# Optimization experiments

Hardware: AMD Instinct MI355X
Metric: run time of the kernel (lower is better)

## Reference

```python
import jax, jax.numpy as jnp
import numpy as np

KEY_CH = 256

def _conv1x1(w, b, t):
    # 1x1 conv with BN folded: t [B,Cin,N] -> [B,Cout,N]
    return jnp.einsum('oc,bcn->bon', w, t) + b[None, :, None]

def _conv1x1_relu(w, b, t):
    return jax.nn.relu(_conv1x1(w, b, t))

def setup_inputs() -> dict:
    key = jax.random.key(0)
    ks = jax.random.split(key, 12)
    B, C, H, W = 4, 512, 128, 128
    d = {}
    d['feat'] = jax.random.normal(ks[0], (B, C, H, W), jnp.float32)
    d['prob'] = jax.random.normal(ks[1], (B, 20, H, W), jnp.float32)  # unused by forward (overwritten)
    s = 0.02
    d['wp1'] = jax.random.normal(ks[2], (KEY_CH, C), jnp.float32) * s
    d['bp1'] = jnp.zeros((KEY_CH,), jnp.float32)
    d['wp2'] = jax.random.normal(ks[3], (KEY_CH, KEY_CH), jnp.float32) * s
    d['bp2'] = jnp.zeros((KEY_CH,), jnp.float32)
    d['wo1'] = jax.random.normal(ks[4], (KEY_CH, C), jnp.float32) * s
    d['bo1'] = jnp.zeros((KEY_CH,), jnp.float32)
    d['wo2'] = jax.random.normal(ks[5], (KEY_CH, KEY_CH), jnp.float32) * s
    d['bo2'] = jnp.zeros((KEY_CH,), jnp.float32)
    d['wd'] = jax.random.normal(ks[6], (KEY_CH, C), jnp.float32) * s
    d['bd'] = jnp.zeros((KEY_CH,), jnp.float32)
    d['wu'] = jax.random.normal(ks[7], (C, KEY_CH), jnp.float32) * s
    d['bu'] = jnp.zeros((C,), jnp.float32)
    d['wout'] = jax.random.normal(ks[8], (512, 2 * C), jnp.float32) * s
    d['bout'] = jnp.zeros((512,), jnp.float32)
    return d


def reference(feat, prob, wp1, bp1, wp2, bp2, wo1, bo1, wo2, bo2, wd, bd, wu, bu, wout, bout):
    B, C, H, W = feat.shape
    x = feat.reshape(B, C, H * W)  # [B,C,N]
    # prob = upsample_bilinear(feat, (H,W)) == feat (identity resize); prob arg is dead.
    # SpatialGather (scale=1): softmax over spatial, weighted pool of features.
    pw = jax.nn.softmax(x, axis=-1)                     # [B,K,N], K == C here
    context = jnp.einsum('bkn,bcn->bck', pw, x)         # [B,C,K] proxy features
    # ObjectAttentionBlock2D
    q = _conv1x1_relu(wp2, bp2, _conv1x1_relu(wp1, bp1, x))        # [B,key,N]
    k = _conv1x1_relu(wo2, bo2, _conv1x1_relu(wo1, bo1, context))  # [B,key,K]
    v = _conv1x1_relu(wd, bd, context)                             # [B,key,K]
    sim = jnp.einsum('bdn,bdk->bnk', q, k) * (KEY_CH ** -0.5)      # [B,N,K]
    sim = jax.nn.softmax(sim, axis=-1)
    ctx = jnp.einsum('bnk,bdk->bdn', sim, v)                       # [B,key,N]
    ctx = _conv1x1_relu(wu, bu, ctx)                               # [B,C,N]
    # SpatialOCR: concat + 1x1 conv + BN + ReLU (dropout identity at eval)
    out = _conv1x1_relu(wout, bout, jnp.concatenate([ctx, x], axis=1))  # [B,out,N]
    return out.reshape(B, -1, H, W)
```

## Files before the change

### kernel.cpp

```cpp
#include <hip/hip_runtime.h>

typedef unsigned int u32;
typedef unsigned short u16;
typedef short s16x8 __attribute__((ext_vector_type(8)));
typedef float f32x4 __attribute__((ext_vector_type(4)));

__device__ __forceinline__ u16 f2bf(float f) {
  u32 u = __float_as_uint(f);
  u32 r = (u + 0x7fffu + ((u >> 16) & 1u)) >> 16;
  return (u16)r;
}

template <int MODE>
__device__ __forceinline__ uint4 pack8(const float* p, float2 st) {
  float4 f0 = *(const float4*)p;
  float4 f1 = *(const float4*)(p + 4);
  float v[8] = {f0.x, f0.y, f0.z, f0.w, f1.x, f1.y, f1.z, f1.w};
  if (MODE == 2) {
#pragma unroll
    for (int j = 0; j < 8; ++j) v[j] = __expf(v[j] - st.x) * st.y;
  }
  uint4 o;
  o.x = (u32)f2bf(v[0]) | ((u32)f2bf(v[1]) << 16);
  o.y = (u32)f2bf(v[2]) | ((u32)f2bf(v[3]) << 16);
  o.z = (u32)f2bf(v[4]) | ((u32)f2bf(v[5]) << 16);
  o.w = (u32)f2bf(v[6]) | ((u32)f2bf(v[7]) << 16);
  return o;
}

__device__ __forceinline__ void g2l16(u16* lds, const u16* g) {
  __builtin_amdgcn_global_load_lds(
      (const __attribute__((address_space(1))) void*)g,
      (__attribute__((address_space(3))) void*)lds, 16, 0, 0);
}

__global__ __launch_bounds__(256) void row_softmax_bf16(
    const float* __restrict__ feat, u16* __restrict__ expx,
    u16* __restrict__ xbf) {
  const long long row = blockIdx.x;
  const float* xp = feat + row * 16384;
  const int tid = threadIdx.x, wv = tid >> 6, ln = tid & 63;
  __shared__ float red[4];
  float4 v[16];
  float mx = -1e30f;
#pragma unroll
  for (int p = 0; p < 16; ++p) {
    v[p] = *(const float4*)(xp + tid * 4 + p * 1024);
    mx = fmaxf(mx, fmaxf(fmaxf(v[p].x, v[p].y), fmaxf(v[p].z, v[p].w)));
  }
  u16* bp = xbf + row * 16384;
#pragma unroll
  for (int p = 0; p < 16; ++p) {
    uint2 ow;
    ow.x = (u32)f2bf(v[p].x) | ((u32)f2bf(v[p].y) << 16);
    ow.y = (u32)f2bf(v[p].z) | ((u32)f2bf(v[p].w) << 16);
    *(uint2*)(bp + tid * 4 + p * 1024) = ow;
  }
  for (int o = 32; o; o >>= 1) mx = fmaxf(mx, __shfl_xor(mx, o, 64));
  if (!ln) red[wv] = mx;
  __syncthreads();
  mx = fmaxf(fmaxf(red[0], red[1]), fmaxf(red[2], red[3]));
  __syncthreads();
  float s = 0.f;
#pragma unroll
  for (int p = 0; p < 16; ++p) {
    v[p].x = __expf(v[p].x - mx);
    v[p].y = __expf(v[p].y - mx);
    v[p].z = __expf(v[p].z - mx);
    v[p].w = __expf(v[p].w - mx);
    s += v[p].x + v[p].y + v[p].z + v[p].w;
  }
  for (int o = 32; o; o >>= 1) s += __shfl_xor(s, o, 64);
  if (!ln) red[wv] = s;
  __syncthreads();
  const float inv = 1.f / (red[0] + red[1] + red[2] + red[3]);
  u16* op = expx + row * 16384;
#pragma unroll
  for (int p = 0; p < 16; ++p) {
    uint2 ow;
    ow.x = (u32)f2bf(v[p].x * inv) | ((u32)f2bf(v[p].y * inv) << 16);
    ow.y = (u32)f2bf(v[p].z * inv) | ((u32)f2bf(v[p].w * inv) << 16);
    *(uint2*)(op + tid * 4 + p * 1024) = ow;
  }
}

__global__ __launch_bounds__(256) void transpose_x(const u16* __restrict__ xbf,
                                                   u16* __restrict__ catT) {
  __shared__ u16 t[32][33];
  const int b = blockIdx.z;
  const int c0 = blockIdx.y << 5, n0 = blockIdx.x << 5;
  const int tx = threadIdx.x & 31, ty = threadIdx.x >> 5;
  const u16* fb = xbf + (long long)b * 512 * 16384;
#pragma unroll
  for (int i = 0; i < 32; i += 8)
    t[ty + i][tx] = fb[(long long)(c0 + ty + i) * 16384 + n0 + tx];
  __syncthreads();
  u16* ob = catT + (long long)b * 16384 * 1024 + 512;
#pragma unroll
  for (int i = 0; i < 32; i += 8)
    ob[(long long)(n0 + ty + i) * 1024 + c0 + tx] = t[tx][ty + i];
}

__global__ __launch_bounds__(256) void cvt_weights(
    const float* __restrict__ w0, const float* __restrict__ w1,
    const float* __restrict__ w2, const float* __restrict__ w3,
    const float* __restrict__ w4, const float* __restrict__ w5,
    const float* __restrict__ w6, u16* __restrict__ dst) {
  const long long i = (long long)blockIdx.x * 256 + threadIdx.x;
  const float* s;
  long long off;
  if (i < 131072) { s = w0; off = 0; }
  else if (i < 196608) { s = w1; off = 131072; }
  else if (i < 327680) { s = w2; off = 196608; }
  else if (i < 393216) { s = w3; off = 327680; }
  else if (i < 524288) { s = w4; off = 393216; }
  else if (i < 655360) { s = w5; off = 524288; }
  else { s = w6; off = 655360; }
  dst[i] = f2bf(s[i - off]);
}

template <int ACT, int BIAS, int SPLITK, int F32OUT>
__global__ __launch_bounds__(512, 1) void gemm256_nt(
    const u16* __restrict__ A, long long sA, int lda,
    const u16* __restrict__ B, long long sB, int ldb,
    void* __restrict__ C, long long sC, int ldc,
    const float* __restrict__ bias, int K, int kchunk) {
  __shared__ __align__(16) u16 As[2][256 * 64];
  __shared__ __align__(16) u16 Bs[2][256 * 64];
  const int tid = threadIdx.x;
  const int wid = tid >> 6, ln = tid & 63;
  const int bz = blockIdx.z;
  const int batch = SPLITK ? (bz >> SPLITK) : bz;
  const int chunk = SPLITK ? (bz & ((1 << SPLITK) - 1)) : 0;
  const long long tm = (long long)blockIdx.y << 8;
  const long long tn = (long long)blockIdx.x << 8;
  const int srow = wid * 8 + (ln >> 3);
  const int scl = ((ln & 7) ^ (ln >> 3)) << 3;
  const long long koff = SPLITK ? (long long)chunk * kchunk : 0;
  const u16* Ab = A + (long long)batch * sA + koff + scl;
  const u16* Bb = B + (long long)batch * sB + koff + scl;
  const u16* rA[4];
  const u16* rB[4];
#pragma unroll
  for (int s = 0; s < 4; ++s) {
    rA[s] = Ab + (tm + s * 64 + srow) * (long long)lda;
    rB[s] = Bb + (tn + s * 64 + srow) * (long long)ldb;
  }
  auto stage = [&](int buf, int kk) {
#pragma unroll
    for (int s = 0; s < 4; ++s) {
      g2l16(&As[buf][s * 4096 + wid * 512], rA[s] + kk);
      g2l16(&Bs[buf][s * 4096 + wid * 512], rB[s] + kk);
    }
  };
  const int fr = ln & 15, fq = ln >> 4;
  const int wm8 = wid >> 2;
  const int wn8 = wid & 3;
  const int arow = (wm8 * 128 + fr) * 64;
  const int brow = (wn8 * 64 + fr) * 64;
  const int ax = fr & 7;
  const int c0 = ((fq ^ ax) << 3);
  const int c1 = c0 ^ 32;
  f32x4 acc[8][4] = {};
  const int nt = (SPLITK ? kchunk : K) >> 6;
  stage(0, 0);
  asm volatile("s_waitcnt vmcnt(0)" ::: "memory");
  asm volatile("s_barrier" ::: "memory");
  for (int t = 0; t < nt; ++t) {
    const int cur = t & 1;
    if (t + 1 < nt) stage(cur ^ 1, (t + 1) << 6);
    s16x8 bfr[4][2];
#pragma unroll
    for (int nf = 0; nf < 4; ++nf) {
      bfr[nf][0] = *(const s16x8*)&Bs[cur][brow + nf * 1024 + c0];
      bfr[nf][1] = *(const s16x8*)&Bs[cur][brow + nf * 1024 + c1];
    }
#pragma unroll
    for (int ph = 0; ph < 4; ++ph) {
      s16x8 a0k0 = *(const s16x8*)&As[cur][arow + (2 * ph) * 1024 + c0];
      s16x8 a0k1 = *(const s16x8*)&As[cur][arow + (2 * ph) * 1024 + c1];
      s16x8 a1k0 = *(const s16x8*)&As[cur][arow + (2 * ph + 1) * 1024 + c0];
      s16x8 a1k1 = *(const s16x8*)&As[cur][arow + (2 * ph + 1) * 1024 + c1];
      __builtin_amdgcn_s_setprio(1);
#pragma unroll
      for (int nf = 0; nf < 4; ++nf) {
        acc[2 * ph][nf] = __builtin_amdgcn_mfma_f32_16x16x32_bf16(
            a0k0, bfr[nf][0], acc[2 * ph][nf], 0, 0, 0);
        acc[2 * ph][nf] = __builtin_amdgcn_mfma_f32_16x16x32_bf16(
            a0k1, bfr[nf][1], acc[2 * ph][nf], 0, 0, 0);
        acc[2 * ph + 1][nf] = __builtin_amdgcn_mfma_f32_16x16x32_bf16(
            a1k0, bfr[nf][0], acc[2 * ph + 1][nf], 0, 0, 0);
        acc[2 * ph + 1][nf] = __builtin_amdgcn_mfma_f32_16x16x32_bf16(
            a1k1, bfr[nf][1], acc[2 * ph + 1][nf], 0, 0, 0);
      }
      __builtin_amdgcn_s_setprio(0);
    }
    if (t + 1 < nt) {
      asm volatile("s_waitcnt vmcnt(0)" ::: "memory");
      asm volatile("s_barrier" ::: "memory");
    }
  }
#pragma unroll
  for (int mf = 0; mf < 8; ++mf) {
    const long long gr0 = tm + wm8 * 128 + mf * 16 + fq * 4;
#pragma unroll
    for (int nf = 0; nf < 4; ++nf) {
      const long long gc = tn + wn8 * 64 + nf * 16 + fr;
      float bc = 0.f;
      if (BIAS == 2) bc = bias[gc];
#pragma unroll
      for (int t = 0; t < 4; ++t) {
        float v = acc[mf][nf][t];
        if (BIAS == 1) v += bias[gr0 + t];
        if (BIAS == 2) v += bc;
        if (ACT) v = fmaxf(v, 0.f);
        const long long idx = (long long)batch * sC + (gr0 + t) * ldc + gc;
        if (SPLITK)
          atomicAdd((float*)C + idx, v);
        else if (F32OUT)
          ((float*)C)[idx] = v;
        else
          ((u16*)C)[idx] = f2bf(v);
      }
    }
  }
}

template <int ACT, int BIAS, int SPLITK, int AMODE, int BMODE, int F32OUT>
__global__ __launch_bounds__(256, 4) void gemm_nt(
    const void* __restrict__ Av, long long sA, int lda,
    const void* __restrict__ Bv, long long sB, int ldb,
    void* __restrict__ C, long long sC, int ldc,
    const float* __restrict__ bias, int K, int kchunk,
    const float2* __restrict__ stats, int statsStride) {
  __shared__ __align__(16) u16 Asm_[2][128 * 32];
  __shared__ __align__(16) u16 Bsm_[2][128 * 32];
  const int tid = threadIdx.x;
  const int wv = tid >> 6;
  const int ln = tid & 63;
  const int bz = blockIdx.z;
  const int batch = SPLITK ? (bz >> 3) : bz;
  const int chunk = SPLITK ? (bz & 7) : 0;
  const long long tm = (long long)blockIdx.y << 7;
  const long long tn = (long long)blockIdx.x << 7;
  const int lrow = ln >> 2;
  const int lcol = (((ln & 3) ^ ((ln >> 3) & 3)) << 3);
  const int w32 = wv << 5;
  const long long ar0 = tm + w32 + lrow, ar1 = ar0 + 16;
  const long long br0 = tn + w32 + lrow, br1 = br0 + 16;
  const long long koff = (long long)chunk * kchunk + lcol;
  const u16* gau0 = (const u16*)Av + (long long)batch * sA + koff + ar0 * lda;
  const u16* gau1 = (const u16*)Av + (long long)batch * sA + koff + ar1 * lda;
  const u16* gbu0 = (const u16*)Bv + (long long)batch * sB + koff + br0 * ldb;
  const u16* gbu1 = (const u16*)Bv + (long long)batch * sB + koff + br1 * ldb;
  const int fr = ln & 15;
  const int fq = ln >> 4;
  const int wm = (wv >> 1) << 6;
  const int wn = (wv & 1) << 6;
  const int rx = (fq ^ ((fr >> 1) & 3)) << 3;
  f32x4 acc[4][4] = {};
  auto stage = [&](int bo, int kk) {
    g2l16(&Asm_[0][bo + w32 * 32], gau0 + kk);
    g2l16(&Asm_[0][bo + w32 * 32 + 512], gau1 + kk);
    g2l16(&Bsm_[0][bo + w32 * 32], gbu0 + kk);
    g2l16(&Bsm_[0][bo + w32 * 32 + 512], gbu1 + kk);
  };
  stage(0, 0);
  asm volatile("s_waitcnt vmcnt(0)" ::: "memory");
  asm volatile("s_barrier" ::: "memory");
  int cb = 0;
  for (int kk = 0; kk < K; kk += 32) {
    s16x8 af[4], bfr[4];
#pragma unroll
    for (int i = 0; i < 4; ++i)
      af[i] = *(const s16x8*)&Asm_[0][cb + (wm + i * 16 + fr) * 32 + rx];
#pragma unroll
    for (int j = 0; j < 4; ++j)
      bfr[j] = *(const s16x8*)&Bsm_[0][cb + (wn + j * 16 + fr) * 32 + rx];
    if (kk + 32 < K) stage(cb ^ 4096, kk + 32);
#pragma unroll
    for (int i = 0; i < 4; ++i)
#pragma unroll
      for (int j = 0; j < 4; ++j)
        acc[i][j] = __builtin_amdgcn_mfma_f32_16x16x32_bf16(
            af[i], bfr[j], acc[i][j], 0, 0, 0);
    __builtin_amdgcn_sched_barrier(0);
    asm volatile("s_waitcnt vmcnt(0) lgkmcnt(0)" ::: "memory");
    asm volatile("s_barrier" ::: "memory");
    cb ^= 4096;
  }
#pragma unroll
  for (int i = 0; i < 4; ++i) {
    const long long gr0 = tm + wm + i * 16 + fq * 4;
#pragma unroll
    for (int j = 0; j < 4; ++j) {
      const long long gc = tn + wn + j * 16 + fr;
      float bc = 0.f;
      if (BIAS == 2) bc = bias[gc];
#pragma unroll
      for (int t = 0; t < 4; ++t) {
        float v = acc[i][j][t];
        if (BIAS == 1) v += bias[gr0 + t];
        if (BIAS == 2) v += bc;
        if (ACT) v = fmaxf(v, 0.f);
        const long long idx = (long long)batch * sC + (gr0 + t) * ldc + gc;
        if (SPLITK)
          atomicAdd((float*)C + idx, v);
        else if (F32OUT)
          ((float*)C)[idx] = v;
        else
          ((u16*)C)[idx] = f2bf(v);
      }
    }
  }
}

__global__ __launch_bounds__(256) void cvt_f32_bf16(const float* __restrict__ s,
                                                    u16* __restrict__ d) {
  const int i = blockIdx.x * 256 + threadIdx.x;
  d[i] = f2bf(s[i]);
}

__global__ __launch_bounds__(256) void softmax_p(u16* __restrict__ P) {
  const int wv = threadIdx.x >> 6, ln = threadIdx.x & 63;
  const long long row = (long long)blockIdx.x * 4 + wv;
  u16* rp = P + row * 1024;
  uint4 r = *(const uint4*)(rp + ln * 8);
  u32 w[4] = {r.x, r.y, r.z, r.w};
  float v[8];
#pragma unroll
  for (int k = 0; k < 4; ++k) {
    v[2 * k] = __uint_as_float(w[k] << 16) * 0.0625f;
    v[2 * k + 1] = __uint_as_float(w[k] & 0xffff0000u) * 0.0625f;
  }
  float m = v[0];
#pragma unroll
  for (int t = 1; t < 8; ++t) m = fmaxf(m, v[t]);
  for (int o = 32; o; o >>= 1) m = fmaxf(m, __shfl_xor(m, o, 64));
  float e[8], s = 0.f;
#pragma unroll
  for (int t = 0; t < 8; ++t) {
    e[t] = __expf(v[t] - m);
    s += e[t];
  }
  for (int o = 32; o; o >>= 1) s += __shfl_xor(s, o, 64);
  const float inv = 1.f / s;
  u32 ow[4];
#pragma unroll
  for (int k = 0; k < 4; ++k)
    ow[k] = (u32)f2bf(e[2 * k] * inv) | ((u32)f2bf(e[2 * k + 1] * inv) << 16);
  *(uint4*)(rp + ln * 8) = make_uint4(ow[0], ow[1], ow[2], ow[3]);
}

extern "C" void kernel_launch(void* const* d_in, const int* in_sizes, int n_in,
                              void* d_out, int out_size, void* d_ws, size_t ws_size,
                              hipStream_t stream) {
  const float* feat = (const float*)d_in[0];
  const float* wp1 = (const float*)d_in[2];
  const float* bp1 = (const float*)d_in[3];
  const float* wp2 = (const float*)d_in[4];
  const float* bp2 = (const float*)d_in[5];
  const float* wo1 = (const float*)d_in[6];
  const float* bo1 = (const float*)d_in[7];
  const float* wo2 = (const float*)d_in[8];
  const float* bo2 = (const float*)d_in[9];
  const float* wd = (const float*)d_in[10];
  const float* bd = (const float*)d_in[11];
  const float* wu = (const float*)d_in[12];
  const float* bu = (const float*)d_in[13];
  const float* wout = (const float*)d_in[14];
  const float* bout = (const float*)d_in[15];
  float* outp = (float*)d_out;
  char* ws = (char*)d_ws;

  u16* catT = (u16*)ws;
  u16* expx = (u16*)(ws + 134217728LL);
  u16* q1T = (u16*)(ws + 134217728LL);
  u16* ctxT = q1T;
  u16* qT = (u16*)(ws + 167772160LL);
  float* ctxF = (float*)(ws + 201326592LL);
  u16* wb = (u16*)(ws + 201326592LL);
  u16* conT = (u16*)(ws + 205520896LL);
  u16* k1hT = (u16*)(ws + 207618048LL);
  u16* kTm = (u16*)(ws + 208666624LL);
  u16* vm = (u16*)(ws + 209715200LL);
  if (ws_size < 210763776ULL) return;
  u16* xbf = (u16*)d_out;
  u16* wp1b = wb + 0;
  u16* wp2b = wb + 131072;
  u16* wo1b = wb + 196608;
  u16* wo2b = wb + 327680;
  u16* wdb = wb + 393216;
  u16* wub = wb + 524288;
  u16* woutb = wb + 655360;

  row_softmax_bf16<<<2048, 256, 0, stream>>>(feat, expx, xbf);
  transpose_x<<<dim3(512, 16, 4), 256, 0, stream>>>(xbf, catT);
  hipMemsetAsync(ctxF, 0, 4194304, stream);
  gemm256_nt<0, 0, 4, 0><<<dim3(2, 2, 64), 512, 0, stream>>>(
      expx, 8388608LL, 16384, xbf, 8388608LL, 16384, ctxF, 262144LL, 512,
      nullptr, 16384, 1024);
  cvt_f32_bf16<<<4096, 256, 0, stream>>>(ctxF, conT);
  cvt_weights<<<4608, 256, 0, stream>>>(wp1, wp2, wo1, wo2, wd, wu, wout, wb);
  gemm_nt<1, 2, 0, 0, 0, 0><<<dim3(2, 4, 4), 256, 0, stream>>>(
      conT, 262144LL, 512, wo1b, 0LL, 512, k1hT, 131072LL, 256, bo1, 512, 0,
      nullptr, 0);
  gemm_nt<1, 2, 0, 0, 0, 0><<<dim3(2, 4, 4), 256, 0, stream>>>(
      k1hT, 131072LL, 256, wo2b, 0LL, 256, kTm, 131072LL, 256, bo2, 256, 0,
      nullptr, 0);
  gemm_nt<1, 1, 0, 0, 0, 0><<<dim3(4, 2, 4), 256, 0, stream>>>(
      wdb, 0LL, 512, conT, 262144LL, 512, vm, 131072LL, 512, bd, 512, 0,
      nullptr, 0);
  gemm256_nt<1, 2, 0, 0><<<dim3(1, 64, 4), 512, 0, stream>>>(
      catT + 512, 16777216LL, 1024, wp1b, 0LL, 512, q1T, 4194304LL, 256, bp1,
      512, 0);
  gemm256_nt<1, 2, 0, 0><<<dim3(1, 64, 4), 512, 0, stream>>>(
      q1T, 4194304LL, 256, wp2b, 0LL, 256, qT, 4194304LL, 256, bp2, 256, 0);
  gemm256_nt<0, 0, 0, 0><<<dim3(2, 64, 4), 512, 0, stream>>>(
      qT, 4194304LL, 256, kTm, 131072LL, 256, catT, 16777216LL, 1024, nullptr,
      256, 0);
  softmax_p<<<16384, 256, 0, stream>>>(catT);
  gemm256_nt<0, 0, 0, 0><<<dim3(1, 64, 4), 512, 0, stream>>>(
      catT, 16777216LL, 1024, vm, 131072LL, 512, ctxT, 4194304LL, 256, nullptr,
      512, 0);
  gemm256_nt<1, 2, 0, 0><<<dim3(2, 64, 4), 512, 0, stream>>>(
      ctxT, 4194304LL, 256, wub, 0LL, 256, catT, 16777216LL, 1024, bu, 256, 0);
  gemm256_nt<1, 1, 0, 1><<<dim3(64, 2, 4), 512, 0, stream>>>(
      woutb, 0LL, 1024, catT, 16777216LL, 1024, outp, 8388608LL, 16384, bout,
      1024, 0);
}
```

Before: 669.0 us.

## Prefetch two K-tiles ahead with partial vmcnt waits in GEMM main loop

Restructures the GEMM main loop to keep two global-to-LDS tile loads in flight, waiting only on the older batch with vmcnt(8) instead of draining all loads each iteration. All A/B fragments are read from LDS into registers first, then a barrier frees the buffer so the load two tiles ahead can be issued before the MFMA block. This aims to hide global load latency behind compute, at the cost of more registers for the A fragments and an extra barrier per iteration.

```diff
diff --git a/kernel.cpp b/kernel.cpp
--- a/kernel.cpp
+++ b/kernel.cpp
@@ -164,41 +164,41 @@
   f32x4 acc[8][4] = {};
   const int nt = (SPLITK ? kchunk : K) >> 6;
   stage(0, 0);
-  asm volatile("s_waitcnt vmcnt(0)" ::: "memory");
-  asm volatile("s_barrier" ::: "memory");
-  for (int t = 0; t < nt; ++t) {
-    const int cur = t & 1;
-    if (t + 1 < nt) stage(cur ^ 1, (t + 1) << 6);
-    s16x8 bfr[4][2];
+  if (nt > 1) stage(1, 64);
+  for (int kt = 0; kt < nt; ++kt) {
+    const int cur = kt & 1;
+    if (kt + 1 < nt)
+      asm volatile("s_waitcnt vmcnt(8)" ::: "memory");
+    else
+      asm volatile("s_waitcnt vmcnt(0)" ::: "memory");
+    asm volatile("s_barrier" ::: "memory");
+    s16x8 bfr[4][2], afr[8][2];
 #pragma unroll
     for (int nf = 0; nf < 4; ++nf) {
       bfr[nf][0] = *(const s16x8*)&Bs[cur][brow + nf * 1024 + c0];
       bfr[nf][1] = *(const s16x8*)&Bs[cur][brow + nf * 1024 + c1];
     }
 #pragma unroll
-    for (int ph = 0; ph < 4; ++ph) {
-      s16x8 a0k0 = *(const s16x8*)&As[cur][arow + (2 * ph) * 1024 + c0];
-      s16x8 a0k1 = *(const s16x8*)&As[cur][arow + (2 * ph) * 1024 + c1];
-      s16x8 a1k0 = *(const s16x8*)&As[cur][arow + (2 * ph + 1) * 1024 + c0];
-      s16x8 a1k1 = *(const s16x8*)&As[cur][arow + (2 * ph + 1) * 1024 + c1];
-      __builtin_amdgcn_s_setprio(1);
+    for (int mf = 0; mf < 8; ++mf) {
+      afr[mf][0] = *(const s16x8*)&As[cur][arow + mf * 1024 + c0];
+      afr[mf][1] = *(const s16x8*)&As[cur][arow + mf * 1024 + c1];
+    }
+    __builtin_amdgcn_sched_barrier(0);
+    asm volatile("s_waitcnt lgkmcnt(0)" ::: "memory");
+    asm volatile("s_barrier" ::: "memory");
+    if (kt + 2 < nt) stage(cur, (kt + 2) << 6);
+    __builtin_amdgcn_sched_barrier(0);
+    __builtin_amdgcn_s_setprio(1);
+#pragma unroll
+    for (int mf = 0; mf < 8; ++mf)
 #pragma unroll
       for (int nf = 0; nf < 4; ++nf) {
-        acc[2 * ph][nf] = __builtin_amdgcn_mfma_f32_16x16x32_bf16(
-            a0k0, bfr[nf][0], acc[2 * ph][nf], 0, 0, 0);
-        acc[2 * ph][nf] = __builtin_amdgcn_mfma_f32_16x16x32_bf16(
-            a0k1, bfr[nf][1], acc[2 * ph][nf], 0, 0, 0);
-        acc[2 * ph + 1][nf] = __builtin_amdgcn_mfma_f32_16x16x32_bf16(
-            a1k0, bfr[nf][0], acc[2 * ph + 1][nf], 0, 0, 0);
-        acc[2 * ph + 1][nf] = __builtin_amdgcn_mfma_f32_16x16x32_bf16(
-            a1k1, bfr[nf][1], acc[2 * ph + 1][nf], 0, 0, 0);
+        acc[mf][nf] = __builtin_amdgcn_mfma_f32_16x16x32_bf16(
+            afr[mf][0], bfr[nf][0], acc[mf][nf], 0, 0, 0);
+        acc[mf][nf] = __builtin_amdgcn_mfma_f32_16x16x32_bf16(
+            afr[mf][1], bfr[nf][1], acc[mf][nf], 0, 0, 0);
       }
-      __builtin_amdgcn_s_setprio(0);
-    }
-    if (t + 1 < nt) {
-      asm volatile("s_waitcnt vmcnt(0)" ::: "memory");
-      asm volatile("s_barrier" ::: "memory");
-    }
+    __builtin_amdgcn_s_setprio(0);
   }
 #pragma unroll
   for (int mf = 0; mf < 8; ++mf) {
```

After: 645.5 us. -3.5%, faster.
